# Kernel tuning notes

Measured on AMD Instinct MI355X. Metric: run time of the kernel, lower is better.

The kernel has to match this reference:

```python
import jax, jax.numpy as jnp
import numpy as np

D_MODEL, D_STATE, L = 512, 64, 1024
BATCH = 8


def setup_inputs() -> dict:
    key = jax.random.key(0)
    ks = jax.random.split(key, 8)
    dt_min, dt_max = 1e-3, 1e-1
    log_dt = jax.random.uniform(ks[0], (D_MODEL,)) * (np.log(dt_max) - np.log(dt_min)) + np.log(dt_min)
    log_A_real = jnp.log(0.5 * jnp.ones((D_MODEL, D_STATE)))
    A_imag = jnp.pi * jnp.tile(jnp.arange(D_STATE, dtype=jnp.float32), (D_MODEL, 1))
    B_real = jnp.ones((D_MODEL, D_STATE), jnp.float32)
    B_imag = jnp.zeros((D_MODEL, D_STATE), jnp.float32)
    C_real = jax.random.normal(ks[1], (D_MODEL, D_STATE))
    C_imag = jax.random.normal(ks[2], (D_MODEL, D_STATE))
    D = jax.random.normal(ks[3], (D_MODEL,))
    # 1x1 conv (Conv1d kernel_size=1) -> weight (2H, H), bias (2H,)
    conv_w = jax.random.normal(ks[4], (2 * D_MODEL, D_MODEL)) / np.sqrt(D_MODEL)
    conv_b = jnp.zeros((2 * D_MODEL,), jnp.float32)
    dec_w = jax.random.normal(ks[5], (1, D_MODEL)) / np.sqrt(D_MODEL)
    dec_b = jnp.zeros((1,), jnp.float32)
    u = jax.random.normal(ks[6], (BATCH, D_MODEL, L))
    return dict(u=u, log_dt=log_dt, log_A_real=log_A_real, A_imag=A_imag,
                B_real=B_real, B_imag=B_imag, C_real=C_real, C_imag=C_imag,
                D=D, conv_w=conv_w, conv_b=conv_b, dec_w=dec_w, dec_b=dec_b)


def _s4d_kernel(log_dt, log_A_real, A_imag, B_real, B_imag, C_real, C_imag, Lk):
    dt = jnp.exp(log_dt)                              # (H,)
    A = -jnp.exp(log_A_real) + 1j * A_imag            # (H, N) complex
    dtA = A * dt[:, None]                             # (H, N)
    A_bar = jnp.exp(dtA)
    Bc = B_real + 1j * B_imag
    B_bar = (A_bar - 1.0) / A * Bc                    # ZOH discretization
    Cc = C_real + 1j * C_imag
    t = jnp.arange(Lk)                                # (L,)
    # A_bar^t = exp(dtA * t); fuse C*B_bar weighting, reduce over state N
    A_pow = jnp.exp(dtA[:, :, None] * t)              # (H, N, L)
    K = jnp.einsum('hn,hnl->hl', Cc * B_bar, A_pow)   # (H, L) complex
    return K.real


def reference(u, log_dt, log_A_real, A_imag, B_real, B_imag, C_real, C_imag,
              D, conv_w, conv_b, dec_w, dec_b):
    H, Lk = u.shape[1], u.shape[2]
    K = _s4d_kernel(log_dt, log_A_real, A_imag, B_real, B_imag, C_real, C_imag, Lk)
    # depthwise cross-correlation (torch conv1d semantics), padding L-1, keep first L
    y = jax.lax.conv_general_dilated(
        u, K[:, None, :], window_strides=(1,), padding=[(Lk - 1, Lk - 1)],
        feature_group_count=H, dimension_numbers=('NCH', 'OIH', 'NCH'))
    y = y[:, :, :Lk]
    y = y + u * D[:, None]
    y = jax.nn.gelu(y, approximate=False)
    # 1x1 conv + GLU over channel dim
    z = jnp.einsum('oc,bcl->bol', conv_w, y) + conv_b[:, None]
    a, b = jnp.split(z, 2, axis=1)
    y = a * jax.nn.sigmoid(b)                         # (B, H, L)
    pooled = y.mean(axis=-1)                          # (B, H)
    return pooled @ dec_w.T + dec_b                   # (B, 1)
```

## Files before the change

kernel.cpp:

```cpp
#include <hip/hip_runtime.h>
#include <hip/hip_bf16.h>
#include <math.h>

typedef __attribute__((ext_vector_type(8))) short short8;
typedef __attribute__((ext_vector_type(4))) float f32x4;
typedef __attribute__((ext_vector_type(16))) float f32x16;
typedef __attribute__((ext_vector_type(4))) unsigned int uint4v;

constexpr int Hm = 512, Lm = 1024, Bm = 8;

static __device__ __forceinline__ unsigned short f2bf(float f) {
    __hip_bfloat16 h = __float2bfloat16(f);
    return *reinterpret_cast<unsigned short*>(&h);
}
static __device__ __forceinline__ float bf2f(unsigned short u) {
    return __uint_as_float((unsigned)u << 16);
}
static __device__ __forceinline__ uint2 pack4(const unsigned short* x) {
    return make_uint2((unsigned)x[0] | ((unsigned)x[1] << 16),
                      (unsigned)x[2] | ((unsigned)x[3] << 16));
}
static __device__ __forceinline__ short8 ld16u(const char* p) {
    uint2 a = *(const uint2*)p;
    uint2 b = *(const uint2*)(p + 8);
    uint4v t = { a.x, a.y, b.x, b.y };
    return __builtin_bit_cast(short8, t);
}

__global__ __launch_bounds__(256, 2) void k_tconv(const float* __restrict__ log_dt,
                                                  const float* __restrict__ log_A_real,
                                                  const float* __restrict__ A_imag,
                                                  const float* __restrict__ B_real,
                                                  const float* __restrict__ B_imag,
                                                  const float* __restrict__ C_real,
                                                  const float* __restrict__ C_imag,
                                                  const float* __restrict__ conv_w,
                                                  const float* __restrict__ u,
                                                  const float* __restrict__ Dvec,
                                                  unsigned short* __restrict__ Woh,
                                                  unsigned short* __restrict__ YbfH) {
    __shared__ __align__(16) char smem[36160];
    const int tid = threadIdx.x, lane = tid & 63, w = tid >> 6;
    const int h = blockIdx.x;
    const int m = lane & 31, q = lane >> 5;
    const int cg = (lane >> 3) & 3, b = lane & 7;
    float* Kf = (float*)(smem + 8800);
    float* pl = (float*)(smem + 12896);

    {
        int i = h * 1024 + tid * 4;
        float4 v = *(const float4*)&conv_w[i];
        *(uint2*)&Woh[i] = make_uint2((unsigned)f2bf(v.x) | ((unsigned)f2bf(v.y) << 16),
                                      (unsigned)f2bf(v.z) | ((unsigned)f2bf(v.w) << 16));
    }
    if (tid < 64) {
        int idx = h * 64 + tid;
        double dt = exp((double)log_dt[h]);
        double Ar = -exp((double)log_A_real[idx]);
        double Ai = (double)A_imag[idx];
        double ar = Ar * dt, ai = Ai * dt;
        double er = exp(ar);
        double rr = er * cos(ai), ri = er * sin(ai);
        double nr = rr - 1.0, ni = ri;
        double den = Ar * Ar + Ai * Ai;
        double qr = (nr * Ar + ni * Ai) / den;
        double qi = (ni * Ar - nr * Ai) / den;
        double Br = (double)B_real[idx], Bi = (double)B_imag[idx];
        double bbr = qr * Br - qi * Bi, bbi = qr * Bi + qi * Br;
        double Cr = (double)C_real[idx], Ci = (double)C_imag[idx];
        double wr = Cr * bbr - Ci * bbi, wi = Cr * bbi + Ci * bbr;
        double e64 = exp(ar * 64.0);
        double p64 = ai * 64.0;
        pl[0 * 64 + tid] = (float)rr;
        pl[1 * 64 + tid] = (float)ri;
        pl[2 * 64 + tid] = (float)wr;
        pl[3 * 64 + tid] = (float)wi;
        pl[4 * 64 + tid] = (float)(e64 * cos(p64));
        pl[5 * 64 + tid] = (float)(e64 * sin(p64));
    }
    __syncthreads();

    {
        float* kl = (float*)(smem + 17600) + w * 1056;
        const float rrf = pl[0 * 64 + lane], rif = pl[1 * 64 + lane];
        float pr = pl[2 * 64 + lane], pi = pl[3 * 64 + lane];
        float br = pl[4 * 64 + lane], bi = pl[5 * 64 + lane];
        int cc = w * 4;
        while (cc) {
            if (cc & 1) { float t_ = pr * br - pi * bi; pi = fmaf(pr, bi, pi * br); pr = t_; }
            float t2 = br * br - bi * bi; bi = 2.f * br * bi; br = t2;
            cc >>= 1;
        }
        const int jj = lane & 15, nq = lane >> 4;
        for (int qq = 0; qq < 16; ++qq) {
            #pragma unroll
            for (int j = 0; j < 16; ++j) {
                kl[j * 66 + lane] = pr;
                float t_ = pr * rrf - pi * rif; pi = fmaf(pr, rif, pi * rrf); pr = t_;
            }
            asm volatile("s_waitcnt lgkmcnt(0)" ::: "memory");
            float s0 = 0.f, s1 = 0.f;
            #pragma unroll
            for (int n = 0; n < 16; n += 4) {
                float2 a = *(const float2*)&kl[jj * 66 + nq * 16 + n];
                float2 b2 = *(const float2*)&kl[jj * 66 + nq * 16 + n + 2];
                s0 += a.x + a.y; s1 += b2.x + b2.y;
            }
            float s = s0 + s1;
            s += __shfl_xor(s, 16);
            s += __shfl_xor(s, 32);
            if (lane < 16) Kf[w * 256 + qq * 16 + jj] = s;
            asm volatile("s_waitcnt lgkmcnt(0)" ::: "memory");
        }
    }
    __syncthreads();

    {
        unsigned int* Gd = (unsigned int*)smem;
        for (int t = tid; t < 2200; t += 256) {
            int s = t / 550;
            int d = t - s * 550;
            int idx0 = 2 * d + s;
            float k0 = (idx0 < 1024) ? Kf[idx0] : 0.f;
            float k1 = (idx0 + 1 < 1024) ? Kf[idx0 + 1] : 0.f;
            Gd[t] = (unsigned)f2bf(k0) | ((unsigned)f2bf(k1) << 16);
        }
    }
    if (tid < 8) { uint4 z = {0, 0, 0, 0}; ((uint4*)(smem + 36032))[tid] = z; }
    __syncthreads();

    {
        const int b2 = tid >> 5, t32 = tid & 31;
        const float* ub = u + ((size_t)(b2 * 512 + h)) * 1024;
        #pragma unroll
        for (int g = 0; g < 8; ++g) {
            int s = t32 * 4 + g * 128;
            float4 v = *(const float4*)&ub[s];
            unsigned short t0 = f2bf(v.x), t1 = f2bf(v.y), t2 = f2bf(v.z), t3 = f2bf(v.w);
            int jc = s >> 6, e = s & 63;
            *(uint2*)(smem + 17600 + jc * 1152 + b2 * 144 + e * 2) =
                make_uint2((unsigned)t0 | ((unsigned)t1 << 16),
                           (unsigned)t2 | ((unsigned)t3 << 16));
        }
    }
    __syncthreads();

    const int icg = (cg == 0) ? w : (cg == 1) ? 7 - w : (cg == 2) ? 8 + w : 15 - w;
    const int dmax = 15 - w;

    int aU = 17600 + icg * 1152 + b * 144 + q * 16;
    const int zl = 36032 + q * 16;

    const int r = (3 - m) & 3;
    int baseH = r * 2200 + (991 - m - r + 8 * q) * 2;

    const f32x16 zacc = {};
    f32x16 acc0 = zacc, acc1 = zacc;

    short8 m2, m1, w0, w1, w2, w3;
    {
        const char* pH = smem + baseH;
        m2 = ld16u(pH +   0); m1 = ld16u(pH +  32);
        w0 = ld16u(pH +  64); w1 = ld16u(pH +  96);
        w2 = ld16u(pH + 128); w3 = ld16u(pH + 160);
    }

    for (int d = 0; d <= dmax; ++d) {
        const char* pb = smem + ((d <= icg) ? aU : zl);
        short8 b0 = *(const short8*)(pb +  0);
        short8 b1 = *(const short8*)(pb + 32);
        short8 b2 = *(const short8*)(pb + 64);
        short8 b3 = *(const short8*)(pb + 96);
        acc0 = __builtin_amdgcn_mfma_f32_32x32x16_bf16(w0, b0, acc0, 0, 0, 0);
        acc1 = __builtin_amdgcn_mfma_f32_32x32x16_bf16(m2, b0, acc1, 0, 0, 0);
        acc0 = __builtin_amdgcn_mfma_f32_32x32x16_bf16(w1, b1, acc0, 0, 0, 0);
        acc1 = __builtin_amdgcn_mfma_f32_32x32x16_bf16(m1, b1, acc1, 0, 0, 0);
        acc0 = __builtin_amdgcn_mfma_f32_32x32x16_bf16(w2, b2, acc0, 0, 0, 0);
        acc1 = __builtin_amdgcn_mfma_f32_32x32x16_bf16(w0, b2, acc1, 0, 0, 0);
        acc0 = __builtin_amdgcn_mfma_f32_32x32x16_bf16(w3, b3, acc0, 0, 0, 0);
        acc1 = __builtin_amdgcn_mfma_f32_32x32x16_bf16(w1, b3, acc1, 0, 0, 0);
        baseH -= 128; aU -= 1152;
        if (d < dmax) {
            const char* pH = smem + baseH;
            m2 = ld16u(pH +   0); m1 = ld16u(pH +  32);
            w0 = ld16u(pH +  64); w1 = ld16u(pH +  96);
            w2 = ld16u(pH + 128); w3 = ld16u(pH + 160);
        }
    }

    const float Dh = Dvec[h];
    __syncthreads();

    #pragma unroll
    for (int mf = 0; mf < 2; ++mf) {
        const f32x16 ac = mf ? acc1 : acc0;
        #pragma unroll
        for (int rq = 0; rq < 4; ++rq) {
            const int row0 = mf * 32 + 8 * rq + 4 * q;
            uint2 uv2 = *(const uint2*)(smem + 17600 + icg * 1152 + b * 144 + row0 * 2);
            unsigned short us[4] = { (unsigned short)(uv2.x & 0xffff),
                                     (unsigned short)(uv2.x >> 16),
                                     (unsigned short)(uv2.y & 0xffff),
                                     (unsigned short)(uv2.y >> 16) };
            unsigned short oh[4];
            #pragma unroll
            for (int k = 0; k < 4; ++k) {
                float y = ac[rq * 4 + k] + Dh * bf2f(us[k]);
                float g = 0.5f * y * (1.0f + erff(y * 0.70710678118654752f));
                oh[k] = f2bf(g);
            }
            *(uint2*)(smem + icg * 1088 + b * 136 + row0 * 2) = pack4(oh);
        }
    }
    __syncthreads();
    {
        const int b2 = tid >> 5, t32 = tid & 31;
        unsigned short* dst = YbfH + ((size_t)(b2 * 512 + h)) * 1024;
        #pragma unroll
        for (int g = 0; g < 8; ++g) {
            int s = t32 * 4 + g * 128;
            int jc = s >> 6, e = s & 63;
            uint2 v = *(const uint2*)(smem + jc * 1088 + b2 * 136 + e * 2);
            *(uint2*)&dst[s] = v;
        }
    }
}

__global__ __launch_bounds__(256) void k2_gemm(const unsigned short* __restrict__ WbfH,
                                               const unsigned short* __restrict__ Ybf,
                                               const float* __restrict__ conv_b,
                                               const float* __restrict__ dec_w,
                                               float* __restrict__ partial) {
    __shared__ unsigned short WTh[128][40];
    __shared__ unsigned short YT[128][44];
    __shared__ float red[4][64][20];
    const int tid = threadIdx.x, lane = tid & 63, wid = tid >> 6;
    const int b = blockIdx.z, oblk = blockIdx.y, lblk = blockIdx.x;
    const int o0 = oblk * 64, l0 = lblk * 128;
    const int fr = lane & 15, fq = lane >> 4;

    f32x4 acc[8][2] = {};

    const int srow = tid >> 1, skh = (tid & 1) * 16;
    const int grow = (srow < 64) ? (o0 + srow) : (512 + o0 + srow - 64);
    const size_t woff = (size_t)grow * 512 + skh;
    const int cp = tid & 15, lg = tid >> 4;

    for (int c0 = 0; c0 < 512; c0 += 32) {
        __syncthreads();
        uint4 wh0 = *(const uint4*)(WbfH + woff + c0);
        uint4 wh1 = *(const uint4*)(WbfH + woff + c0 + 8);
        const unsigned short* ys0 = Ybf + ((size_t)(b * 512 + c0 + 2 * cp)) * 1024 + l0 + lg * 8;
        uint4 y0 = *(const uint4*)ys0;
        uint4 y1 = *(const uint4*)(ys0 + 1024);
        *(uint4*)&WTh[srow][skh]     = wh0;
        *(uint4*)&WTh[srow][skh + 8] = wh1;
        {
            const unsigned int* a = (const unsigned int*)&y0;
            const unsigned int* c = (const unsigned int*)&y1;
            #pragma unroll
            for (int t2 = 0; t2 < 4; ++t2) {
                unsigned int lo = (a[t2] & 0xffffu) | (c[t2] << 16);
                unsigned int hi = (a[t2] >> 16) | (c[t2] & 0xffff0000u);
                *(unsigned int*)&YT[lg * 8 + 2 * t2][2 * cp] = lo;
                *(unsigned int*)&YT[lg * 8 + 2 * t2 + 1][2 * cp] = hi;
            }
        }
        __syncthreads();
        short8 b0h = ld16u((const char*)&YT[wid * 32 + fr][fq * 8]);
        short8 b1h = ld16u((const char*)&YT[wid * 32 + 16 + fr][fq * 8]);
        #pragma unroll
        for (int mf = 0; mf < 8; ++mf) {
            short8 ah = *(const short8*)&WTh[mf * 16 + fr][fq * 8];
            acc[mf][0] = __builtin_amdgcn_mfma_f32_16x16x32_bf16(ah, b0h, acc[mf][0], 0, 0, 0);
            acc[mf][1] = __builtin_amdgcn_mfma_f32_16x16x32_bf16(ah, b1h, acc[mf][1], 0, 0, 0);
        }
    }

    #pragma unroll
    for (int mf = 0; mf < 4; ++mf)
        #pragma unroll
        for (int j = 0; j < 4; ++j) {
            int ol = mf * 16 + fq * 4 + j;
            float ba = conv_b[o0 + ol];
            float bb = conv_b[512 + o0 + ol];
            float s = 0.f;
            #pragma unroll
            for (int nf = 0; nf < 2; ++nf) {
                float za = acc[mf][nf][j] + ba;
                float zb = acc[mf + 4][nf][j] + bb;
                s += za / (1.f + expf(-zb));
            }
            red[wid][ol][fr] = s;
        }
    __syncthreads();
    if (tid < 64) {
        float s = 0.f;
        #pragma unroll
        for (int w = 0; w < 4; ++w) {
            float4 r0 = *(const float4*)&red[w][tid][0];
            float4 r1 = *(const float4*)&red[w][tid][4];
            float4 r2 = *(const float4*)&red[w][tid][8];
            float4 r3 = *(const float4*)&red[w][tid][12];
            s += (r0.x + r0.y + r0.z + r0.w) + (r1.x + r1.y + r1.z + r1.w)
               + (r2.x + r2.y + r2.z + r2.w) + (r3.x + r3.y + r3.z + r3.w);
        }
        float val = s * dec_w[o0 + tid] * (1.0f / 1024.0f);
        #pragma unroll
        for (int off = 32; off; off >>= 1) val += __shfl_xor(val, off);
        if (tid == 0) partial[((b * 8) + oblk) * 8 + lblk] = val;
    }
}

__global__ void k3_final(const float* __restrict__ partial,
                         const float* __restrict__ dec_b,
                         float* __restrict__ out) {
    int b = threadIdx.x;
    if (b < Bm) {
        float s = dec_b[0];
        for (int i = 0; i < 64; ++i) s += partial[b * 64 + i];
        out[b] = s;
    }
}

extern "C" void kernel_launch(void* const* d_in, const int* in_sizes, int n_in,
                              void* d_out, int out_size, void* d_ws, size_t ws_size,
                              hipStream_t stream) {
    const float* u          = (const float*)d_in[0];
    const float* log_dt     = (const float*)d_in[1];
    const float* log_A_real = (const float*)d_in[2];
    const float* A_imag     = (const float*)d_in[3];
    const float* B_real     = (const float*)d_in[4];
    const float* B_imag     = (const float*)d_in[5];
    const float* C_real     = (const float*)d_in[6];
    const float* C_imag     = (const float*)d_in[7];
    const float* Dvec       = (const float*)d_in[8];
    const float* conv_w     = (const float*)d_in[9];
    const float* conv_b     = (const float*)d_in[10];
    const float* dec_w      = (const float*)d_in[11];
    const float* dec_b      = (const float*)d_in[12];

    char* base = (char*)d_ws;
    unsigned short* YbfH = (unsigned short*)base;
    unsigned short* Wh   = (unsigned short*)(base + 8388608);
    float* partial       = (float*)(base + 9437184);
    float* out           = (float*)d_out;

    k_tconv<<<512, 256, 0, stream>>>(log_dt, log_A_real, A_imag, B_real, B_imag,
                                     C_real, C_imag, conv_w, u, Dvec, Wh, YbfH);
    k2_gemm<<<dim3(8, 8, 8), 256, 0, stream>>>(Wh, YbfH, conv_b, dec_w, partial);
    k3_final<<<1, 64, 0, stream>>>(partial, dec_b, out);
}
```

Baseline: 56.61 us.

## Prefetch u early, 8-way shifted Toeplitz copies, double-buffer GEMM global loads

In the conv kernel, u is loaded into registers at kernel start so its global latency overlaps the SSM kernel computation. The Toeplitz bf16 K table now holds 8 shifted copies instead of 4, so A-fragment loads become aligned 16-byte LDS reads rather than split 8-byte loads. The GEMM kernel register-prefetches the next chunk of weights and activations before the MMA loop, overlapping global loads with compute. The cost is more LDS (about 42KB), more registers, and a larger table-build loop.

```diff
diff --git a/kernel.cpp b/kernel.cpp
--- a/kernel.cpp
+++ b/kernel.cpp
@@ -39,13 +39,22 @@
                                                   const float* __restrict__ Dvec,
                                                   unsigned short* __restrict__ Woh,
                                                   unsigned short* __restrict__ YbfH) {
-    __shared__ __align__(16) char smem[36160];
+    __shared__ __align__(16) char smem[41984];
     const int tid = threadIdx.x, lane = tid & 63, w = tid >> 6;
     const int h = blockIdx.x;
     const int m = lane & 31, q = lane >> 5;
     const int cg = (lane >> 3) & 3, b = lane & 7;
-    float* Kf = (float*)(smem + 8800);
-    float* pl = (float*)(smem + 12896);
+    float* Kf = (float*)(smem + 36352);
+    float* pl = (float*)(smem + 40448);
+
+    float4 ureg[8];
+    {
+        const int b2 = tid >> 5, t32 = tid & 31;
+        const float* ub = u + ((size_t)(b2 * 512 + h)) * 1024;
+        #pragma unroll
+        for (int g = 0; g < 8; ++g) ureg[g] = *(const float4*)&ub[t32 * 4 + g * 128];
+    }
+    const float Dh = Dvec[h];
 
     {
         int i = h * 1024 + tid * 4;
@@ -81,7 +90,7 @@
     __syncthreads();
 
     {
-        float* kl = (float*)(smem + 17600) + w * 1056;
+        float* kl = (float*)(smem + 17792) + w * 1056;
         const float rrf = pl[0 * 64 + lane], rif = pl[1 * 64 + lane];
         float pr = pl[2 * 64 + lane], pi = pl[3 * 64 + lane];
         float br = pl[4 * 64 + lane], bi = pl[5 * 64 + lane];
@@ -117,28 +126,27 @@
 
     {
         unsigned int* Gd = (unsigned int*)smem;
-        for (int t = tid; t < 2200; t += 256) {
-            int s = t / 550;
-            int d = t - s * 550;
+        for (int t = tid; t < 4448; t += 256) {
+            int s = t / 556;
+            int d = t - s * 556;
             int idx0 = 2 * d + s;
             float k0 = (idx0 < 1024) ? Kf[idx0] : 0.f;
             float k1 = (idx0 + 1 < 1024) ? Kf[idx0 + 1] : 0.f;
             Gd[t] = (unsigned)f2bf(k0) | ((unsigned)f2bf(k1) << 16);
         }
     }
-    if (tid < 8) { uint4 z = {0, 0, 0, 0}; ((uint4*)(smem + 36032))[tid] = z; }
+    if (tid < 8) { uint4 z = {0, 0, 0, 0}; ((uint4*)(smem + 36224))[tid] = z; }
     __syncthreads();
 
     {
         const int b2 = tid >> 5, t32 = tid & 31;
-        const float* ub = u + ((size_t)(b2 * 512 + h)) * 1024;
         #pragma unroll
         for (int g = 0; g < 8; ++g) {
             int s = t32 * 4 + g * 128;
-            float4 v = *(const float4*)&ub[s];
+            float4 v = ureg[g];
             unsigned short t0 = f2bf(v.x), t1 = f2bf(v.y), t2 = f2bf(v.z), t3 = f2bf(v.w);
             int jc = s >> 6, e = s & 63;
-            *(uint2*)(smem + 17600 + jc * 1152 + b2 * 144 + e * 2) =
+            *(uint2*)(smem + 17792 + jc * 1152 + b2 * 144 + e * 2) =
                 make_uint2((unsigned)t0 | ((unsigned)t1 << 16),
                            (unsigned)t2 | ((unsigned)t3 << 16));
         }
@@ -148,22 +156,21 @@
     const int icg = (cg == 0) ? w : (cg == 1) ? 7 - w : (cg == 2) ? 8 + w : 15 - w;
     const int dmax = 15 - w;
 
-    int aU = 17600 + icg * 1152 + b * 144 + q * 16;
-    const int zl = 36032 + q * 16;
-
-    const int r = (3 - m) & 3;
-    int baseH = r * 2200 + (991 - m - r + 8 * q) * 2;
+    int aU = 17792 + icg * 1152 + b * 144 + q * 16;
+    const int zl = 36224 + q * 16;
+
+    const int sA = (7 - m) & 7;
+    int baseH = sA * 2224 + (991 - m - sA + 8 * q) * 2;
 
     const f32x16 zacc = {};
     f32x16 acc0 = zacc, acc1 = zacc;
 
     short8 m2, m1, w0, w1, w2, w3;
-    {
-        const char* pH = smem + baseH;
-        m2 = ld16u(pH +   0); m1 = ld16u(pH +  32);
-        w0 = ld16u(pH +  64); w1 = ld16u(pH +  96);
-        w2 = ld16u(pH + 128); w3 = ld16u(pH + 160);
-    }
+#define LDA() { const char* pH = smem + baseH; \
+        m2 = *(const short8*)(pH +   0); m1 = *(const short8*)(pH +  32); \
+        w0 = *(const short8*)(pH +  64); w1 = *(const short8*)(pH +  96); \
+        w2 = *(const short8*)(pH + 128); w3 = *(const short8*)(pH + 160); }
+    LDA();
 
     for (int d = 0; d <= dmax; ++d) {
         const char* pb = smem + ((d <= icg) ? aU : zl);
@@ -180,15 +187,10 @@
         acc0 = __builtin_amdgcn_mfma_f32_32x32x16_bf16(w3, b3, acc0, 0, 0, 0);
         acc1 = __builtin_amdgcn_mfma_f32_32x32x16_bf16(w1, b3, acc1, 0, 0, 0);
         baseH -= 128; aU -= 1152;
-        if (d < dmax) {
-            const char* pH = smem + baseH;
-            m2 = ld16u(pH +   0); m1 = ld16u(pH +  32);
-            w0 = ld16u(pH +  64); w1 = ld16u(pH +  96);
-            w2 = ld16u(pH + 128); w3 = ld16u(pH + 160);
-        }
-    }
-
-    const float Dh = Dvec[h];
+        if (d < dmax) LDA();
+    }
+#undef LDA
+
     __syncthreads();
 
     #pragma unroll
@@ -197,7 +199,7 @@
         #pragma unroll
         for (int rq = 0; rq < 4; ++rq) {
             const int row0 = mf * 32 + 8 * rq + 4 * q;
-            uint2 uv2 = *(const uint2*)(smem + 17600 + icg * 1152 + b * 144 + row0 * 2);
+            uint2 uv2 = *(const uint2*)(smem + 17792 + icg * 1152 + b * 144 + row0 * 2);
             unsigned short us[4] = { (unsigned short)(uv2.x & 0xffff),
                                      (unsigned short)(uv2.x >> 16),
                                      (unsigned short)(uv2.y & 0xffff),
@@ -245,19 +247,20 @@
     const int grow = (srow < 64) ? (o0 + srow) : (512 + o0 + srow - 64);
     const size_t woff = (size_t)grow * 512 + skh;
     const int cp = tid & 15, lg = tid >> 4;
+    const unsigned short* ysb = Ybf + ((size_t)(b * 512 + 2 * cp)) * 1024 + l0 + lg * 8;
+
+    uint4 wc0 = *(const uint4*)(WbfH + woff);
+    uint4 wc1 = *(const uint4*)(WbfH + woff + 8);
+    uint4 yc0 = *(const uint4*)(ysb);
+    uint4 yc1 = *(const uint4*)(ysb + 1024);
 
     for (int c0 = 0; c0 < 512; c0 += 32) {
         __syncthreads();
-        uint4 wh0 = *(const uint4*)(WbfH + woff + c0);
-        uint4 wh1 = *(const uint4*)(WbfH + woff + c0 + 8);
-        const unsigned short* ys0 = Ybf + ((size_t)(b * 512 + c0 + 2 * cp)) * 1024 + l0 + lg * 8;
-        uint4 y0 = *(const uint4*)ys0;
-        uint4 y1 = *(const uint4*)(ys0 + 1024);
-        *(uint4*)&WTh[srow][skh]     = wh0;
-        *(uint4*)&WTh[srow][skh + 8] = wh1;
+        *(uint4*)&WTh[srow][skh]     = wc0;
+        *(uint4*)&WTh[srow][skh + 8] = wc1;
         {
-            const unsigned int* a = (const unsigned int*)&y0;
-            const unsigned int* c = (const unsigned int*)&y1;
+            const unsigned int* a = (const unsigned int*)&yc0;
+            const unsigned int* c = (const unsigned int*)&yc1;
             #pragma unroll
             for (int t2 = 0; t2 < 4; ++t2) {
                 unsigned int lo = (a[t2] & 0xffffu) | (c[t2] << 16);
@@ -265,6 +268,13 @@
                 *(unsigned int*)&YT[lg * 8 + 2 * t2][2 * cp] = lo;
                 *(unsigned int*)&YT[lg * 8 + 2 * t2 + 1][2 * cp] = hi;
             }
+        }
+        if (c0 + 32 < 512) {
+            wc0 = *(const uint4*)(WbfH + woff + c0 + 32);
+            wc1 = *(const uint4*)(WbfH + woff + c0 + 40);
+            const unsigned short* ysn = ysb + (size_t)(c0 + 32) * 1024;
+            yc0 = *(const uint4*)(ysn);
+            yc1 = *(const uint4*)(ysn + 1024);
         }
         __syncthreads();
         short8 b0h = ld16u((const char*)&YT[wid * 32 + fr][fq * 8]);
```

Result: faster. 54.90 us (-3.0%).
